# Performance work log

Hardware: AMD Instinct MI355X
Metric: run time of the kernel (lower is better)

## Reference

```python
import jax, jax.numpy as jnp
import numpy as np

N = 100000   # nodes
E = 1600000  # edges (avg degree 16)
IN, H, OUT = 128, 128, 64
EPS = 1e-5


def setup_inputs() -> dict:
    key = jax.random.key(0)
    ks = jax.random.split(key, 8)

    def glorot(k, i, o):
        s = 1.0 / np.sqrt(i)
        return jax.random.uniform(k, (i, o), jnp.float32, -s, s)

    return {
        "x": jax.random.normal(ks[0], (N, IN), jnp.float32),
        "edge_index": jax.random.randint(ks[1], (2, E), 0, N, dtype=jnp.int32),
        "W1": glorot(ks[2], IN, H), "b1": jnp.zeros((H,), jnp.float32),
        "g1": jnp.ones((H,), jnp.float32), "be1": jnp.zeros((H,), jnp.float32),
        "W2": glorot(ks[3], H, H), "b2": jnp.zeros((H,), jnp.float32),
        "g2": jnp.ones((H,), jnp.float32), "be2": jnp.zeros((H,), jnp.float32),
        "W3": glorot(ks[4], H, OUT), "b3": jnp.zeros((OUT,), jnp.float32),
    }


def gcn_conv(x, W, b, src, dst):
    # PyG GCNConv: add self-loops, symmetric norm D^-1/2 (A+I) D^-1/2, then x@W, bias after aggregation.
    n = x.shape[0]
    h = x @ W                                   # [N, out]
    deg = jnp.zeros((n,), h.dtype).at[dst].add(1.0) + 1.0  # +1 for self-loop
    dis = jax.lax.rsqrt(deg)                    # deg^-1/2
    coef = dis[src] * dis[dst]                  # per-edge norm
    agg = jnp.zeros_like(h).at[dst].add(h[src] * coef[:, None])
    agg = agg + h * (dis * dis)[:, None]        # self-loop messages
    return agg + b


def batch_norm(x, g, b):
    # BatchNorm1d in training mode: batch statistics over nodes, biased variance.
    m = x.mean(axis=0)
    v = x.var(axis=0)
    return (x - m) * jax.lax.rsqrt(v + EPS) * g + b


def reference(x, edge_index, W1, b1, g1, be1, W2, b2, g2, be2, W3, b3):
    src, dst = edge_index[0], edge_index[1]
    h = gcn_conv(x, W1, b1, src, dst)
    h = batch_norm(h, g1, be1)
    h = gcn_conv(h, W2, b2, src, dst)
    h = batch_norm(h, g2, be2)
    out = gcn_conv(h, W3, b3, src, dst)
    return out
```

## Files before the change

kernel.cpp:

```cpp
#include <hip/hip_runtime.h>
#include <hip/hip_fp16.h>


constexpr int BSH = 7;
constexpr int NXCD = 8;

typedef _Float16 half8 __attribute__((ext_vector_type(8)));
typedef float f32x4 __attribute__((ext_vector_type(4)));

static __device__ inline ushort f2h(float f) {
    union { __half h; ushort u; } cv;
    cv.h = __float2half_rn(f);
    return cv.u;
}
static __device__ inline float2 h2f2(unsigned int u) {
    union { unsigned int u; __half2 h; } cv;
    cv.u = u;
    return __half22float2(cv.h);
}

#define ACC8(base, v) do { float2 _f; \
    _f = h2f2((v).x); acc[(base)+0] += _f.x; acc[(base)+1] += _f.y; \
    _f = h2f2((v).y); acc[(base)+2] += _f.x; acc[(base)+3] += _f.y; \
    _f = h2f2((v).z); acc[(base)+4] += _f.x; acc[(base)+5] += _f.y; \
    _f = h2f2((v).w); acc[(base)+6] += _f.x; acc[(base)+7] += _f.y; \
} while (0)

__global__ __launch_bounds__(256) void count_k(const int* __restrict__ dst,
                                               int* __restrict__ hist,
                                               int E, int EPB, int nbuk) {
    __shared__ int lh[1024];
    for (int i = threadIdx.x; i < nbuk; i += 256) lh[i] = 0;
    __syncthreads();
    const int e0 = blockIdx.x * EPB;
    const int e1 = min(e0 + EPB, E);
    for (int e = e0 + threadIdx.x; e < e1; e += 256)
        atomicAdd(&lh[dst[e] >> BSH], 1);
    __syncthreads();
    const int xcd = blockIdx.x & (NXCD - 1);
    for (int i = threadIdx.x; i < nbuk; i += 256) {
        int v = lh[i];
        if (v) atomicAdd(&hist[xcd * nbuk + i], v);
    }
}

__global__ __launch_bounds__(256) void scan_hist_k(const int* __restrict__ hist,
                                                   int* __restrict__ cur,
                                                   int* __restrict__ bstart,
                                                   int* __restrict__ row_ptr,
                                                   float* __restrict__ stats,
                                                   int nbuk, int n, int E) {
    stats[threadIdx.x] = 0.f;
    const int NT = nbuk * NXCD;
    const int C = (NT + 255) / 256;
    int vals[32];
    const int tid = threadIdx.x;
    int sum = 0;
#pragma unroll
    for (int k = 0; k < 32; ++k) {
        if (k >= C) break;
        int key = tid * C + k;
        int v = 0;
        if (key < NT) {
            int b = key >> 3, x = key & 7;
            v = hist[x * nbuk + b];
        }
        vals[k] = v;
        sum += v;
    }
    __shared__ int part[256];
    part[tid] = sum;
    __syncthreads();
    for (int off = 1; off < 256; off <<= 1) {
        int t = 0;
        if (tid >= off) t = part[tid - off];
        __syncthreads();
        part[tid] += t;
        __syncthreads();
    }
    int run = (tid == 0) ? 0 : part[tid - 1];
#pragma unroll
    for (int k = 0; k < 32; ++k) {
        if (k >= C) break;
        int key = tid * C + k;
        if (key < NT) {
            int b = key >> 3, x = key & 7;
            cur[x * nbuk + b] = run;
            if (x == 0) bstart[b] = run;
        }
        run += vals[k];
    }
    if (tid == 0) { bstart[nbuk] = E; row_ptr[n] = E; }
}

__global__ __launch_bounds__(256) void scatter_bucket_k(const int* __restrict__ src,
                                                        const int* __restrict__ dst,
                                                        int* __restrict__ cur,
                                                        unsigned int* __restrict__ ebuf,
                                                        int E, int EPB, int nbuk) {
    __shared__ int lh[1024];
    __shared__ int base[1024];
    for (int i = threadIdx.x; i < nbuk; i += 256) lh[i] = 0;
    __syncthreads();
    const int e0 = blockIdx.x * EPB;
    const int e1 = min(e0 + EPB, E);
    const int xcd = blockIdx.x & (NXCD - 1);
    for (int e = e0 + threadIdx.x; e < e1; e += 256)
        atomicAdd(&lh[dst[e] >> BSH], 1);
    __syncthreads();
    for (int i = threadIdx.x; i < nbuk; i += 256) {
        int v = lh[i];
        base[i] = v ? atomicAdd(&cur[xcd * nbuk + i], v) : 0;
        lh[i] = 0;
    }
    __syncthreads();
    for (int e = e0 + threadIdx.x; e < e1; e += 256) {
        int d = dst[e];
        int s = src[e];
        int b = d >> BSH;
        int pos = base[b] + atomicAdd(&lh[b], 1);
        ebuf[pos] = ((unsigned int)s << BSH) | (unsigned int)(d & 127);
    }
}

__global__ __launch_bounds__(256) void bucket_sort_k(const unsigned int* __restrict__ ebuf,
                                                     const int* __restrict__ bstart,
                                                     int* __restrict__ row_ptr,
                                                     int* __restrict__ esrc, int n) {
    const int b = blockIdx.x;
    const int beg = bstart[b];
    const int end = bstart[b + 1];
    __shared__ int cnt[128], off[128];
    if (threadIdx.x < 128) cnt[threadIdx.x] = 0;
    __syncthreads();
    for (int i = beg + threadIdx.x; i < end; i += 256)
        atomicAdd(&cnt[ebuf[i] & 127], 1);
    __syncthreads();
    if (threadIdx.x < 128) off[threadIdx.x] = cnt[threadIdx.x];
    __syncthreads();
    for (int d = 1; d < 128; d <<= 1) {
        int t = 0;
        if (threadIdx.x < 128 && threadIdx.x >= d) t = off[threadIdx.x - d];
        __syncthreads();
        if (threadIdx.x < 128) off[threadIdx.x] += t;
        __syncthreads();
    }
    if (threadIdx.x < 128) {
        int ex = off[threadIdx.x] - cnt[threadIdx.x];
        int node = (b << BSH) + threadIdx.x;
        if (node < n) row_ptr[node] = beg + ex;
        cnt[threadIdx.x] = ex;
    }
    __syncthreads();
    for (int i = beg + threadIdx.x; i < end; i += 256) {
        unsigned int p = ebuf[i];
        int l = (int)(p & 127);
        int pos = beg + atomicAdd(&cnt[l], 1);
        esrc[pos] = (int)(p >> BSH);
    }
}

__global__ void rowptr_to_dis_k(const int* __restrict__ row_ptr,
                                float* __restrict__ dis, int n) {
    int i = blockIdx.x * blockDim.x + threadIdx.x;
    if (i < n) {
        int deg = row_ptr[i + 1] - row_ptr[i];
        dis[i] = rsqrtf((float)deg + 1.0f);
    }
}

__global__ __launch_bounds__(256) void prep_wt_k(const float* __restrict__ W1,
                                                 const float* __restrict__ W2,
                                                 const float* __restrict__ W3,
                                                 ushort* __restrict__ wt1,
                                                 ushort* __restrict__ wt2,
                                                 ushort* __restrict__ wt3) {
    const float* W; ushort* WT; int OUTD;
    if (blockIdx.x == 0)      { W = W1; WT = wt1; OUTD = 128; }
    else if (blockIdx.x == 1) { W = W2; WT = wt2; OUTD = 128; }
    else                      { W = W3; WT = wt3; OUTD = 64; }
    const int tot = 128 * OUTD;
    for (int idx = threadIdx.x; idx < tot; idx += 256) {
        int nq = idx >> 7;
        int k  = idx & 127;
        WT[idx] = f2h(W[k * OUTD + nq]);
    }
}

template <int OUTD, bool BNIN>
__global__ __launch_bounds__(256) void gemm_reg_k(const float* __restrict__ X,
                                                  const ushort* __restrict__ WT,
                                                  const float* __restrict__ scale,
                                                  const float* __restrict__ shift,
                                                  const float* __restrict__ dis,
                                                  ushort* __restrict__ Hs, int nn) {
    constexpr int NCT = OUTD / 16;
    const int wave = threadIdx.x >> 6;
    const int lane = threadIdx.x & 63;
    const int l15 = lane & 15;
    const int kg = lane >> 4;
    const int row = blockIdx.x * 64 + wave * 16 + l15;

    half8 a[4];
#pragma unroll
    for (int kk = 0; kk < 4; ++kk) {
        if (row < nn) {
            const float4* xp = (const float4*)(X + (size_t)row * 128 + kk * 32 + kg * 8);
            float4 v0 = xp[0];
            float4 v1 = xp[1];
            if (BNIN) {
                int kq = kk * 8 + kg * 2;
                float4 s0 = ((const float4*)scale)[kq];
                float4 s1 = ((const float4*)scale)[kq + 1];
                float4 h0 = ((const float4*)shift)[kq];
                float4 h1 = ((const float4*)shift)[kq + 1];
                v0.x = v0.x * s0.x + h0.x;
                v0.y = v0.y * s0.y + h0.y;
                v0.z = v0.z * s0.z + h0.z;
                v0.w = v0.w * s0.w + h0.w;
                v1.x = v1.x * s1.x + h1.x;
                v1.y = v1.y * s1.y + h1.y;
                v1.z = v1.z * s1.z + h1.z;
                v1.w = v1.w * s1.w + h1.w;
            }
            a[kk][0] = (_Float16)v0.x;
            a[kk][1] = (_Float16)v0.y;
            a[kk][2] = (_Float16)v0.z;
            a[kk][3] = (_Float16)v0.w;
            a[kk][4] = (_Float16)v1.x;
            a[kk][5] = (_Float16)v1.y;
            a[kk][6] = (_Float16)v1.z;
            a[kk][7] = (_Float16)v1.w;
        } else {
#pragma unroll
            for (int j = 0; j < 8; ++j) a[kk][j] = (_Float16)0.f;
        }
    }

    f32x4 acc[NCT];
#pragma unroll
    for (int ct = 0; ct < NCT; ++ct) acc[ct] = (f32x4){0.f, 0.f, 0.f, 0.f};

#pragma unroll
    for (int kk = 0; kk < 4; ++kk) {
#pragma unroll
        for (int ct = 0; ct < NCT; ++ct) {
            half8 bfr = *(const half8*)&WT[(ct * 16 + l15) * 128 + kk * 32 + kg * 8];
            acc[ct] = __builtin_amdgcn_mfma_f32_16x16x32_f16(a[kk], bfr, acc[ct], 0, 0, 0);
        }
    }

    const int mbase = blockIdx.x * 64 + wave * 16 + kg * 4;
    float dm[4];
#pragma unroll
    for (int reg = 0; reg < 4; ++reg) {
        int m = mbase + reg;
        dm[reg] = (m < nn) ? dis[m] : 0.f;
    }
#pragma unroll
    for (int ct = 0; ct < NCT; ++ct) {
        int ncol = ct * 16 + l15;
        size_t cb = (size_t)(ncol >> 5) * nn * 32 + (ncol & 31);
#pragma unroll
        for (int reg = 0; reg < 4; ++reg) {
            int m = mbase + reg;
            if (m < nn) Hs[cb + (size_t)m * 32] = f2h(acc[ct][reg] * dm[reg]);
        }
    }
}

template <int OUTD, bool STATS>
__global__ __launch_bounds__(256) void gather_k(const ushort* __restrict__ Hs,
                                                const float* __restrict__ dis,
                                                const float* __restrict__ b,
                                                const int* __restrict__ row_ptr,
                                                const int* __restrict__ esrc,
                                                float* __restrict__ O,
                                                float* __restrict__ sums,
                                                float* __restrict__ sumsq, int n) {
    constexpr int NCHUNK = OUTD / 32;

    __shared__ float s_sum[32];
    __shared__ float s_sq[32];
    if (STATS) {
        if (threadIdx.x < 32) { s_sum[threadIdx.x] = 0.f; s_sq[threadIdx.x] = 0.f; }
        __syncthreads();
    }

    const int chunk = blockIdx.x & (NCHUNK - 1);
    const int nblk  = blockIdx.x / NCHUNK;
    const int g     = threadIdx.x >> 1;
    const int lane  = threadIdx.x & 1;
    const int node  = nblk * 128 + g;

    float acc[16];
#pragma unroll
    for (int c = 0; c < 16; ++c) acc[c] = 0.f;
    float o[16];
#pragma unroll
    for (int c = 0; c < 16; ++c) o[c] = 0.f;

    if (node < n) {
        const uint4* Hc = (const uint4*)Hs + (size_t)chunk * n * 4;

        {
            uint4 v0 = Hc[(size_t)node * 4 + lane];
            uint4 v1 = Hc[(size_t)node * 4 + lane + 2];
            ACC8(0, v0);
            ACC8(8, v1);
        }
        const int beg = row_ptr[node];
        const int end = row_ptr[node + 1];
        int j = beg;
        const int end8 = beg + ((end - beg) & ~7);
        for (; j < end8; j += 8) {
            int s[8];
#pragma unroll
            for (int u = 0; u < 8; ++u) s[u] = esrc[j + u];
            uint4 va[8], vb[8];
#pragma unroll
            for (int u = 0; u < 8; ++u) va[u] = Hc[(size_t)s[u] * 4 + lane];
#pragma unroll
            for (int u = 0; u < 8; ++u) vb[u] = Hc[(size_t)s[u] * 4 + lane + 2];
#pragma unroll
            for (int u = 0; u < 8; ++u) { ACC8(0, va[u]); }
#pragma unroll
            for (int u = 0; u < 8; ++u) { ACC8(8, vb[u]); }
        }
        for (; j < end; ++j) {
            int s = esrc[j];
            uint4 a = Hc[(size_t)s * 4 + lane];
            uint4 c = Hc[(size_t)s * 4 + lane + 2];
            ACC8(0, a);
            ACC8(8, c);
        }

        float dd = dis[node];
        const float4* B4 = (const float4*)b + chunk * 8 + lane * 2;
        float4 b0 = B4[0];
        float4 b1 = B4[1];
        float4 b2 = B4[4];
        float4 b3 = B4[5];
        o[0]  = acc[0]  * dd + b0.x;
        o[1]  = acc[1]  * dd + b0.y;
        o[2]  = acc[2]  * dd + b0.z;
        o[3]  = acc[3]  * dd + b0.w;
        o[4]  = acc[4]  * dd + b1.x;
        o[5]  = acc[5]  * dd + b1.y;
        o[6]  = acc[6]  * dd + b1.z;
        o[7]  = acc[7]  * dd + b1.w;
        o[8]  = acc[8]  * dd + b2.x;
        o[9]  = acc[9]  * dd + b2.y;
        o[10] = acc[10] * dd + b2.z;
        o[11] = acc[11] * dd + b2.w;
        o[12] = acc[12] * dd + b3.x;
        o[13] = acc[13] * dd + b3.y;
        o[14] = acc[14] * dd + b3.z;
        o[15] = acc[15] * dd + b3.w;

        float4* O4 = (float4*)O + (size_t)node * (OUTD / 4) + chunk * 8 + lane * 2;
        O4[0] = make_float4(o[0], o[1], o[2], o[3]);
        O4[1] = make_float4(o[4], o[5], o[6], o[7]);
        O4[4] = make_float4(o[8], o[9], o[10], o[11]);
        O4[5] = make_float4(o[12], o[13], o[14], o[15]);
    }

    if (STATS) {
        float sv[16], qv[16];
#pragma unroll
        for (int c = 0; c < 16; ++c) { sv[c] = o[c]; qv[c] = o[c] * o[c]; }
#pragma unroll
        for (int c = 0; c < 16; ++c) {
#pragma unroll
            for (int m = 2; m <= 32; m <<= 1) {
                sv[c] += __shfl_xor(sv[c], m);
                qv[c] += __shfl_xor(qv[c], m);
            }
        }
        if ((threadIdx.x & 63) < 2) {
            int c0 = lane * 8;
            int c1 = 16 + lane * 8;
#pragma unroll
            for (int c = 0; c < 8; ++c) {
                atomicAdd(&s_sum[c0 + c], sv[c]);
                atomicAdd(&s_sq[c0 + c], qv[c]);
                atomicAdd(&s_sum[c1 + c], sv[8 + c]);
                atomicAdd(&s_sq[c1 + c], qv[8 + c]);
            }
        }
        __syncthreads();
        if (threadIdx.x < 32) {
            atomicAdd(&sums[chunk * 32 + threadIdx.x], s_sum[threadIdx.x]);
            atomicAdd(&sumsq[chunk * 32 + threadIdx.x], s_sq[threadIdx.x]);
        }
    }
}

__global__ void bn_finalize_k(float* __restrict__ sums, float* __restrict__ sumsq,
                              const float* __restrict__ g, const float* __restrict__ be,
                              float* __restrict__ scale, float* __restrict__ shift, int n) {
    int c = threadIdx.x;
    float inv_n = 1.0f / (float)n;
    float m = sums[c] * inv_n;
    float v = sumsq[c] * inv_n - m * m;
    float sc = rsqrtf(v + 1e-5f) * g[c];
    scale[c] = sc;
    shift[c] = be[c] - m * sc;
    sums[c] = 0.f;
    sumsq[c] = 0.f;
}

extern "C" void kernel_launch(void* const* d_in, const int* in_sizes, int n_in,
                              void* d_out, int out_size, void* d_ws, size_t ws_size,
                              hipStream_t stream) {
    const float* x   = (const float*)d_in[0];
    const int*   ei  = (const int*)d_in[1];
    const float* W1  = (const float*)d_in[2];
    const float* b1  = (const float*)d_in[3];
    const float* g1  = (const float*)d_in[4];
    const float* be1 = (const float*)d_in[5];
    const float* W2  = (const float*)d_in[6];
    const float* b2  = (const float*)d_in[7];
    const float* g2  = (const float*)d_in[8];
    const float* be2 = (const float*)d_in[9];
    const float* W3  = (const float*)d_in[10];
    const float* b3  = (const float*)d_in[11];
    float* out = (float*)d_out;

    const int N = in_sizes[0] / 128;
    const int E = in_sizes[1] / 2;
    const int* src = ei;
    const int* dst = ei + E;
    const int NBUK = (N + 127) >> BSH;

    float* wsp   = (float*)d_ws;
    float* dis   = wsp;
    float* stats = wsp + N;
    ushort* wt1  = (ushort*)(stats + 512);
    ushort* wt2  = wt1 + 128 * 128;
    ushort* wt3  = wt2 + 128 * 128;
    int*   hist   = (int*)(wt3 + 128 * 64);
    int*   cur    = hist + NBUK * NXCD;
    int*   bstart = cur + NBUK * NXCD;
    int*   row_ptr = bstart + NBUK + 1 + 63;
    float* bufA  = (float*)((((uintptr_t)(row_ptr + N + 1)) + 255) & ~(uintptr_t)255);
    float* bufB  = bufA + (size_t)N * 128;
    unsigned int* ebuf = (unsigned int*)(bufB + (size_t)N * 128);
    int*   esrc  = (int*)(ebuf + E);

    ushort* Hs = (ushort*)bufA;

    float* sums  = stats;
    float* sumsq = stats + 128;
    float* scale = stats + 256;
    float* shift = stats + 384;

    const int BS = 256;
    dim3 blk(BS);
    const int NB = (N + 255) / 256;
    const int SGRID = 128;
    const int EPB = (E + SGRID - 1) / SGRID;

    hipMemsetAsync(hist, 0, (size_t)NBUK * NXCD * 4, stream);
    prep_wt_k<<<dim3(3), blk, 0, stream>>>(W1, W2, W3, wt1, wt2, wt3);
    count_k<<<dim3(SGRID), blk, 0, stream>>>(dst, hist, E, EPB, NBUK);
    scan_hist_k<<<dim3(1), blk, 0, stream>>>(hist, cur, bstart, row_ptr, stats, NBUK, N, E);
    scatter_bucket_k<<<dim3(SGRID), blk, 0, stream>>>(src, dst, cur, ebuf, E, EPB, NBUK);
    bucket_sort_k<<<dim3(NBUK), blk, 0, stream>>>(ebuf, bstart, row_ptr, esrc, N);
    rowptr_to_dis_k<<<dim3(NB), blk, 0, stream>>>(row_ptr, dis, N);

    const int gemm_grid = (N + 63) / 64;
    const int NBg = (N + 127) / 128;

    gemm_reg_k<128, false><<<dim3(gemm_grid), blk, 0, stream>>>(x, wt1, nullptr, nullptr,
                                                                dis, Hs, N);
    gather_k<128, true><<<dim3(NBg * 4), blk, 0, stream>>>(Hs, dis, b1, row_ptr, esrc,
                                                           bufB, sums, sumsq, N);
    bn_finalize_k<<<dim3(1), dim3(128), 0, stream>>>(sums, sumsq, g1, be1, scale, shift, N);

    gemm_reg_k<128, true><<<dim3(gemm_grid), blk, 0, stream>>>(bufB, wt2, scale, shift,
                                                               dis, Hs, N);
    gather_k<128, true><<<dim3(NBg * 4), blk, 0, stream>>>(Hs, dis, b2, row_ptr, esrc,
                                                           bufB, sums, sumsq, N);
    bn_finalize_k<<<dim3(1), dim3(128), 0, stream>>>(sums, sumsq, g2, be2, scale, shift, N);

    gemm_reg_k<64, true><<<dim3(gemm_grid), blk, 0, stream>>>(bufB, wt3, scale, shift,
                                                              dis, Hs, N);
    gather_k<64, false><<<dim3(NBg * 2), blk, 0, stream>>>(Hs, dis, b3, row_ptr, esrc,
                                                           out, nullptr, nullptr, N);
}
```

Before: 453.5 us.

## Store intermediate GCN activations in fp16 and use four lanes per node in gather

Gather kernels for layers 1 and 2 now write their output as packed fp16 instead of fp32, and the following GEMM reads fp16 and converts before applying batch-norm scale and shift. This halves the intermediate activation write and read traffic. The gather kernel also changes from 2 lanes per node with 16 accumulators to 4 lanes per node with 8 accumulators, with 64 nodes per block, so there are more threads and fewer registers per thread and each lane makes one 16-byte load per edge. Rounding the pre-BN activations to fp16 adds precision loss, and the BN statistics are still taken from the fp32 values before rounding.

Measured after the change: 429.8 us. -5.2%, faster.

```diff
diff --git a/kernel.cpp b/kernel.cpp
--- a/kernel.cpp
+++ b/kernel.cpp
@@ -19,11 +19,11 @@
     return __half22float2(cv.h);
 }
 
-#define ACC8(base, v) do { float2 _f; \
-    _f = h2f2((v).x); acc[(base)+0] += _f.x; acc[(base)+1] += _f.y; \
-    _f = h2f2((v).y); acc[(base)+2] += _f.x; acc[(base)+3] += _f.y; \
-    _f = h2f2((v).z); acc[(base)+4] += _f.x; acc[(base)+5] += _f.y; \
-    _f = h2f2((v).w); acc[(base)+6] += _f.x; acc[(base)+7] += _f.y; \
+#define ACC8(v) do { float2 _f; \
+    _f = h2f2((v).x); acc[0] += _f.x; acc[1] += _f.y; \
+    _f = h2f2((v).y); acc[2] += _f.x; acc[3] += _f.y; \
+    _f = h2f2((v).z); acc[4] += _f.x; acc[5] += _f.y; \
+    _f = h2f2((v).w); acc[6] += _f.x; acc[7] += _f.y; \
 } while (0)
 
 __global__ __launch_bounds__(256) void count_k(const int* __restrict__ dst,
@@ -187,8 +187,8 @@
     }
 }
 
-template <int OUTD, bool BNIN>
-__global__ __launch_bounds__(256) void gemm_reg_k(const float* __restrict__ X,
+template <int OUTD, bool XF16, bool BNIN>
+__global__ __launch_bounds__(256) void gemm_reg_k(const void* __restrict__ Xv,
                                                   const ushort* __restrict__ WT,
                                                   const float* __restrict__ scale,
                                                   const float* __restrict__ shift,
@@ -204,33 +204,42 @@
     half8 a[4];
 #pragma unroll
     for (int kk = 0; kk < 4; ++kk) {
+        float v[8];
         if (row < nn) {
-            const float4* xp = (const float4*)(X + (size_t)row * 128 + kk * 32 + kg * 8);
-            float4 v0 = xp[0];
-            float4 v1 = xp[1];
+            if (XF16) {
+                const uint4* xp = (const uint4*)((const ushort*)Xv + (size_t)row * 128
+                                                 + kk * 32 + kg * 8);
+                uint4 raw = *xp;
+                float2 f;
+                f = h2f2(raw.x); v[0] = f.x; v[1] = f.y;
+                f = h2f2(raw.y); v[2] = f.x; v[3] = f.y;
+                f = h2f2(raw.z); v[4] = f.x; v[5] = f.y;
+                f = h2f2(raw.w); v[6] = f.x; v[7] = f.y;
+            } else {
+                const float4* xp = (const float4*)((const float*)Xv + (size_t)row * 128
+                                                   + kk * 32 + kg * 8);
+                float4 v0 = xp[0];
+                float4 v1 = xp[1];
+                v[0] = v0.x; v[1] = v0.y; v[2] = v0.z; v[3] = v0.w;
+                v[4] = v1.x; v[5] = v1.y; v[6] = v1.z; v[7] = v1.w;
+            }
             if (BNIN) {
                 int kq = kk * 8 + kg * 2;
                 float4 s0 = ((const float4*)scale)[kq];
                 float4 s1 = ((const float4*)scale)[kq + 1];
                 float4 h0 = ((const float4*)shift)[kq];
                 float4 h1 = ((const float4*)shift)[kq + 1];
-                v0.x = v0.x * s0.x + h0.x;
-                v0.y = v0.y * s0.y + h0.y;
-                v0.z = v0.z * s0.z + h0.z;
-                v0.w = v0.w * s0.w + h0.w;
-                v1.x = v1.x * s1.x + h1.x;
-                v1.y = v1.y * s1.y + h1.y;
-                v1.z = v1.z * s1.z + h1.z;
-                v1.w = v1.w * s1.w + h1.w;
+                v[0] = v[0] * s0.x + h0.x;
+                v[1] = v[1] * s0.y + h0.y;
+                v[2] = v[2] * s0.z + h0.z;
+                v[3] = v[3] * s0.w + h0.w;
+                v[4] = v[4] * s1.x + h1.x;
+                v[5] = v[5] * s1.y + h1.y;
+                v[6] = v[6] * s1.z + h1.z;
+                v[7] = v[7] * s1.w + h1.w;
             }
-            a[kk][0] = (_Float16)v0.x;
-            a[kk][1] = (_Float16)v0.y;
-            a[kk][2] = (_Float16)v0.z;
-            a[kk][3] = (_Float16)v0.w;
-            a[kk][4] = (_Float16)v1.x;
-            a[kk][5] = (_Float16)v1.y;
-            a[kk][6] = (_Float16)v1.z;
-            a[kk][7] = (_Float16)v1.w;
+#pragma unroll
+            for (int j = 0; j < 8; ++j) a[kk][j] = (_Float16)v[j];
         } else {
 #pragma unroll
             for (int j = 0; j < 8; ++j) a[kk][j] = (_Float16)0.f;
@@ -269,13 +278,13 @@
     }
 }
 
-template <int OUTD, bool STATS>
+template <int OUTD, bool STATS, bool OUTF16>
 __global__ __launch_bounds__(256) void gather_k(const ushort* __restrict__ Hs,
                                                 const float* __restrict__ dis,
                                                 const float* __restrict__ b,
                                                 const int* __restrict__ row_ptr,
                                                 const int* __restrict__ esrc,
-                                                float* __restrict__ O,
+                                                void* __restrict__ Ov,
                                                 float* __restrict__ sums,
                                                 float* __restrict__ sumsq, int n) {
     constexpr int NCHUNK = OUTD / 32;
@@ -289,25 +298,23 @@
 
     const int chunk = blockIdx.x & (NCHUNK - 1);
     const int nblk  = blockIdx.x / NCHUNK;
-    const int g     = threadIdx.x >> 1;
-    const int lane  = threadIdx.x & 1;
-    const int node  = nblk * 128 + g;
-
-    float acc[16];
-#pragma unroll
-    for (int c = 0; c < 16; ++c) acc[c] = 0.f;
-    float o[16];
-#pragma unroll
-    for (int c = 0; c < 16; ++c) o[c] = 0.f;
+    const int g     = threadIdx.x >> 2;
+    const int lane  = threadIdx.x & 3;
+    const int node  = nblk * 64 + g;
+
+    float acc[8];
+#pragma unroll
+    for (int c = 0; c < 8; ++c) acc[c] = 0.f;
+    float o[8];
+#pragma unroll
+    for (int c = 0; c < 8; ++c) o[c] = 0.f;
 
     if (node < n) {
         const uint4* Hc = (const uint4*)Hs + (size_t)chunk * n * 4;
 
         {
-            uint4 v0 = Hc[(size_t)node * 4 + lane];
-            uint4 v1 = Hc[(size_t)node * 4 + lane + 2];
-            ACC8(0, v0);
-            ACC8(8, v1);
+            uint4 v = Hc[(size_t)node * 4 + lane];
+            ACC8(v);
         }
         const int beg = row_ptr[node];
         const int end = row_ptr[node + 1];
@@ -317,75 +324,61 @@
             int s[8];
 #pragma unroll
             for (int u = 0; u < 8; ++u) s[u] = esrc[j + u];
-            uint4 va[8], vb[8];
+            uint4 va[8];
 #pragma unroll
             for (int u = 0; u < 8; ++u) va[u] = Hc[(size_t)s[u] * 4 + lane];
 #pragma unroll
-            for (int u = 0; u < 8; ++u) vb[u] = Hc[(size_t)s[u] * 4 + lane + 2];
-#pragma unroll
-            for (int u = 0; u < 8; ++u) { ACC8(0, va[u]); }
-#pragma unroll
-            for (int u = 0; u < 8; ++u) { ACC8(8, vb[u]); }
+            for (int u = 0; u < 8; ++u) { ACC8(va[u]); }
         }
         for (; j < end; ++j) {
             int s = esrc[j];
             uint4 a = Hc[(size_t)s * 4 + lane];
-            uint4 c = Hc[(size_t)s * 4 + lane + 2];
-            ACC8(0, a);
-            ACC8(8, c);
+            ACC8(a);
         }
 
         float dd = dis[node];
         const float4* B4 = (const float4*)b + chunk * 8 + lane * 2;
         float4 b0 = B4[0];
         float4 b1 = B4[1];
-        float4 b2 = B4[4];
-        float4 b3 = B4[5];
-        o[0]  = acc[0]  * dd + b0.x;
-        o[1]  = acc[1]  * dd + b0.y;
-        o[2]  = acc[2]  * dd + b0.z;
-        o[3]  = acc[3]  * dd + b0.w;
-        o[4]  = acc[4]  * dd + b1.x;
-        o[5]  = acc[5]  * dd + b1.y;
-        o[6]  = acc[6]  * dd + b1.z;
-        o[7]  = acc[7]  * dd + b1.w;
-        o[8]  = acc[8]  * dd + b2.x;
-        o[9]  = acc[9]  * dd + b2.y;
-        o[10] = acc[10] * dd + b2.z;
-        o[11] = acc[11] * dd + b2.w;
-        o[12] = acc[12] * dd + b3.x;
-        o[13] = acc[13] * dd + b3.y;
-        o[14] = acc[14] * dd + b3.z;
-        o[15] = acc[15] * dd + b3.w;
-
-        float4* O4 = (float4*)O + (size_t)node * (OUTD / 4) + chunk * 8 + lane * 2;
-        O4[0] = make_float4(o[0], o[1], o[2], o[3]);
-        O4[1] = make_float4(o[4], o[5], o[6], o[7]);
-        O4[4] = make_float4(o[8], o[9], o[10], o[11]);
-        O4[5] = make_float4(o[12], o[13], o[14], o[15]);
+        o[0] = acc[0] * dd + b0.x;
+        o[1] = acc[1] * dd + b0.y;
+        o[2] = acc[2] * dd + b0.z;
+        o[3] = acc[3] * dd + b0.w;
+        o[4] = acc[4] * dd + b1.x;
+        o[5] = acc[5] * dd + b1.y;
+        o[6] = acc[6] * dd + b1.z;
+        o[7] = acc[7] * dd + b1.w;
+
+        if (OUTF16) {
+            union { ushort us[8]; uint4 v; } pk;
+#pragma unroll
+            for (int c = 0; c < 8; ++c) pk.us[c] = f2h(o[c]);
+            ((uint4*)Ov)[(size_t)node * (OUTD / 8) + chunk * 4 + lane] = pk.v;
+        } else {
+            float4* O4 = (float4*)Ov + (size_t)node * (OUTD / 4) + chunk * 8 + lane * 2;
+            O4[0] = make_float4(o[0], o[1], o[2], o[3]);
+            O4[1] = make_float4(o[4], o[5], o[6], o[7]);
+        }
     }
 
     if (STATS) {
-        float sv[16], qv[16];
-#pragma unroll
-        for (int c = 0; c < 16; ++c) { sv[c] = o[c]; qv[c] = o[c] * o[c]; }
-#pragma unroll
-        for (int c = 0; c < 16; ++c) {
-#pragma unroll
-            for (int m = 2; m <= 32; m <<= 1) {
+        float sv[8], qv[8];
+#pragma unroll
+        for (int c = 0; c < 8; ++c) { sv[c] = o[c]; qv[c] = o[c] * o[c]; }
+#pragma unroll
+        for (int c = 0; c < 8; ++c) {
+#pragma unroll
+            for (int m = 4; m <= 32; m <<= 1) {
                 sv[c] += __shfl_xor(sv[c], m);
                 qv[c] += __shfl_xor(qv[c], m);
             }
         }
-        if ((threadIdx.x & 63) < 2) {
+        if ((threadIdx.x & 63) < 4) {
             int c0 = lane * 8;
-            int c1 = 16 + lane * 8;
 #pragma unroll
             for (int c = 0; c < 8; ++c) {
                 atomicAdd(&s_sum[c0 + c], sv[c]);
                 atomicAdd(&s_sq[c0 + c], qv[c]);
-                atomicAdd(&s_sum[c1 + c], sv[8 + c]);
-                atomicAdd(&s_sq[c1 + c], qv[8 + c]);
             }
         }
         __syncthreads();
@@ -448,7 +441,8 @@
     unsigned int* ebuf = (unsigned int*)(bufB + (size_t)N * 128);
     int*   esrc  = (int*)(ebuf + E);
 
-    ushort* Hs = (ushort*)bufA;
+    ushort* Hs  = (ushort*)bufA;
+    ushort* Bf16 = (ushort*)bufB;
 
     float* sums  = stats;
     float* sumsq = stats + 128;
@@ -470,22 +464,22 @@
     rowptr_to_dis_k<<<dim3(NB), blk, 0, stream>>>(row_ptr, dis, N);
 
     const int gemm_grid = (N + 63) / 64;
-    const int NBg = (N + 127) / 128;
-
-    gemm_reg_k<128, false><<<dim3(gemm_grid), blk, 0, stream>>>(x, wt1, nullptr, nullptr,
-                                                                dis, Hs, N);
-    gather_k<128, true><<<dim3(NBg * 4), blk, 0, stream>>>(Hs, dis, b1, row_ptr, esrc,
-                                                           bufB, sums, sumsq, N);
+    const int NBg = (N + 63) / 64;
+
+    gemm_reg_k<128, false, false><<<dim3(gemm_grid), blk, 0, stream>>>(
+        x, wt1, nullptr, nullptr, dis, Hs, N);
+    gather_k<128, true, true><<<dim3(NBg * 4), blk, 0, stream>>>(
+        Hs, dis, b1, row_ptr, esrc, Bf16, sums, sumsq, N);
     bn_finalize_k<<<dim3(1), dim3(128), 0, stream>>>(sums, sumsq, g1, be1, scale, shift, N);
 
-    gemm_reg_k<128, true><<<dim3(gemm_grid), blk, 0, stream>>>(bufB, wt2, scale, shift,
-                                                               dis, Hs, N);
-    gather_k<128, true><<<dim3(NBg * 4), blk, 0, stream>>>(Hs, dis, b2, row_ptr, esrc,
-                                                           bufB, sums, sumsq, N);
+    gemm_reg_k<128, true, true><<<dim3(gemm_grid), blk, 0, stream>>>(
+        Bf16, wt2, scale, shift, dis, Hs, N);
+    gather_k<128, true, true><<<dim3(NBg * 4), blk, 0, stream>>>(
+        Hs, dis, b2, row_ptr, esrc, Bf16, sums, sumsq, N);
     bn_finalize_k<<<dim3(1), dim3(128), 0, stream>>>(sums, sumsq, g2, be2, scale, shift, N);
 
-    gemm_reg_k<64, true><<<dim3(gemm_grid), blk, 0, stream>>>(bufB, wt3, scale, shift,
-                                                              dis, Hs, N);
-    gather_k<64, false><<<dim3(NBg * 2), blk, 0, stream>>>(Hs, dis, b3, row_ptr, esrc,
-                                                           out, nullptr, nullptr, N);
-}
+    gemm_reg_k<64, true, true><<<dim3(gemm_grid), blk, 0, stream>>>(
+        Bf16, wt3, scale, shift, dis, Hs, N);
+    gather_k<64, false, false><<<dim3(NBg * 2), blk, 0, stream>>>(
+        Hs, dis, b3, row_ptr, esrc, out, nullptr, nullptr, N);
+}
```
